# Performance work log

Measured on AMD Instinct MI355X. Metric: run time of the kernel, lower is better.

Reference implementation:

```python
import jax, jax.numpy as jnp
import numpy as np

EPS = 1e-6  # LayerNorm epsilon


def setup_inputs() -> dict:
    key = jax.random.key(0)
    ks = jax.random.split(key, 12)
    B, S, T, E = 8, 2048, 2048, 512
    sc = 1.0 / np.sqrt(E)
    inp = {
        "encoder_outputs": jax.random.normal(ks[0], (B, S, E), jnp.float32),
        "emotion": jax.random.normal(ks[1], (B, T, E), jnp.float32),
        "mask": jax.random.randint(ks[2], (B, S, T), 0, 2).astype(bool),
        "Wq": jax.random.normal(ks[3], (E, E), jnp.float32) * sc,
        "bq": jnp.zeros((E,), jnp.float32),
        "Wk": jax.random.normal(ks[4], (E, E), jnp.float32) * sc,
        "bk": jnp.zeros((E,), jnp.float32),
        "Wv": jax.random.normal(ks[5], (E, E), jnp.float32) * sc,
        "bv": jnp.zeros((E,), jnp.float32),
        "Wo": jax.random.normal(ks[6], (E, E), jnp.float32) * sc,
        "gamma": jnp.ones((E,), jnp.float32),
        "beta": jnp.zeros((E,), jnp.float32),
    }
    return inp


def reference(encoder_outputs, emotion, mask, Wq, bq, Wk, bk, Wv, bv, Wo, gamma, beta):
    # Linear projections (torch Linear: x @ W.T + b)
    q = encoder_outputs @ Wq.T + bq          # [B,S,E]
    k = emotion @ Wk.T + bk                  # [B,T,E]
    v = emotion @ Wv.T + bv                  # [B,T,E]
    logits = jnp.einsum("bse,bte->bst", q, k)  # [B,S,T]
    logits = jnp.where(mask, jnp.float32(-1e18), logits)
    weights = jax.nn.softmax(logits, axis=-1)   # dropout1 = identity (eval)
    contexts = jnp.einsum("bst,bte->bse", weights, v)
    attn = contexts @ Wo.T                   # output_linear, no bias
    attn = encoder_outputs + attn            # dropout2 = identity (eval)
    # LayerNorm (std-based, as in common hand-rolled LayerNorm)
    mean = attn.mean(-1, keepdims=True)
    std = attn.std(-1, keepdims=True)
    context = gamma * (attn - mean) / (std + EPS) + beta
    context = encoder_outputs + context      # dropout3 = identity (eval)
    return context
```

## Files before the change

### kernel.cpp

```cpp
#include <hip/hip_runtime.h>
#include <math.h>
#include <stdint.h>


#define BB 8
#define SS 2048
#define TT 2048
#define EE 512

typedef __attribute__((ext_vector_type(8))) short short8;
typedef __attribute__((ext_vector_type(4))) float f32x4;

__device__ __forceinline__ uint16_t f2bf(float f) {
  uint32_t u = __builtin_bit_cast(uint32_t, f);
  u += 0x7fffu + ((u >> 16) & 1u);
  return (uint16_t)(u >> 16);
}
__device__ __forceinline__ float bf2f(uint16_t h) {
  uint32_t u = ((uint32_t)h) << 16;
  return __builtin_bit_cast(float, u);
}

__device__ __forceinline__ size_t toff(int row, int col, int ld) {
  return (size_t)(row >> 4) * ((size_t)ld << 4) + ((size_t)(col >> 3) << 7)
       + ((row & 15) << 3) + (col & 7);
}

__device__ __forceinline__ void gld16(const void* g, void* l) {
  __builtin_amdgcn_global_load_lds(
      (const __attribute__((address_space(1))) void*)g,
      (__attribute__((address_space(3))) void*)l, 16, 0, 0);
}

template<int ASRC, int BSRC, int EPI, int WN>
__global__ __launch_bounds__(256, 2) void mgemm(
    const void* __restrict__ Ap, const void* __restrict__ Alo,
    const void* __restrict__ Bp, const void* __restrict__ Blo,
    void* __restrict__ Cp, void* __restrict__ C2,
    const float* __restrict__ bias, const float* __restrict__ bias2,
    const float* __restrict__ resid,
    const int* __restrict__ mask, float* __restrict__ sZ,
    int K, int lda, int ldb, int ldc,
    size_t sA, size_t sB, size_t sC, size_t sM)
{
  constexpr bool ALOARR = (ASRC == 0);
  constexpr bool BLOARR = (BSRC == 0);
  constexpr bool T3     = (ASRC == 0) && (BSRC == 0);
  constexpr bool T2     = (ASRC == 0) && (BSRC == 1);
  constexpr int  BN     = 32 * WN;
  constexpr int  ABYTES = ALOARR ? 16384 : 8192;
  constexpr int  BBYTES = BLOARR ? BN * 128 : BN * 64;

  __shared__ char smem[ABYTES + BBYTES];

  const int tid  = threadIdx.x;
  const int lane = tid & 63, wv = tid >> 6;
  const int z    = blockIdx.z;
  const int bm   = blockIdx.y * 128;
  const int bn   = blockIdx.x * BN;
  const int fr   = lane & 15;
  const int wm   = (wv & 1) * 64;
  const int wn   = (wv >> 1) * (16 * WN);

  const f32x4 zero = {0.f, 0.f, 0.f, 0.f};
  f32x4 acc[4][WN];
#pragma unroll
  for (int i = 0; i < 4; ++i)
#pragma unroll
    for (int j = 0; j < WN; ++j) acc[i][j] = zero;

  const size_t loff = (size_t)lane * 8;
  const uint16_t* gAh = (const uint16_t*)Ap + sA * z + (size_t)(bm >> 4) * 16 * lda + loff;
  const uint16_t* gAl = ALOARR ? (const uint16_t*)Alo + sA * z + (size_t)(bm >> 4) * 16 * lda + loff : nullptr;
  const uint16_t* gBh = (const uint16_t*)Bp + sB * z + (size_t)(bn >> 4) * 16 * ldb + loff;
  const uint16_t* gBl = BLOARR ? (const uint16_t*)Blo + sB * z + (size_t)(bn >> 4) * 16 * ldb + loff : nullptr;

  for (int k0 = 0; k0 < K; k0 += 32) {
    const size_t ka = (size_t)k0 * 16;
    __syncthreads();
#pragma unroll
    for (int t = 0; t < 2; ++t) { int s = wv + t * 4;
      gld16(gAh + (size_t)s * 16 * lda + ka, &smem[s * 1024]); }
    if constexpr (ALOARR) {
#pragma unroll
      for (int t = 0; t < 2; ++t) { int s = wv + t * 4;
        gld16(gAl + (size_t)s * 16 * lda + ka, &smem[8192 + s * 1024]); }
    }
#pragma unroll
    for (int t = 0; t < WN / 2; ++t) { int s = wv + t * 4;
      gld16(gBh + (size_t)s * 16 * ldb + ka, &smem[ABYTES + s * 1024]); }
    if constexpr (BLOARR) {
#pragma unroll
      for (int t = 0; t < WN / 2; ++t) { int s = wv + t * 4;
        gld16(gBl + (size_t)s * 16 * ldb + ka, &smem[ABYTES + BN * 64 + s * 1024]); }
    }
    __syncthreads();

    short8 ah[4], bh[WN], al_[4], bl_[WN];
#pragma unroll
    for (int i = 0; i < 4; ++i) {
      const char* p = smem + ((wm >> 4) + i) * 1024 + (lane << 4);
      ah[i] = *(const short8*)p;
      if constexpr (ALOARR) al_[i] = *(const short8*)(p + 8192);
    }
#pragma unroll
    for (int j = 0; j < WN; ++j) {
      const char* p = smem + ABYTES + ((wn >> 4) + j) * 1024 + (lane << 4);
      bh[j] = *(const short8*)p;
      if constexpr (BLOARR) bl_[j] = *(const short8*)(p + BN * 64);
    }
#pragma unroll
    for (int i = 0; i < 4; ++i)
#pragma unroll
      for (int j = 0; j < WN; ++j) {
        acc[i][j] = __builtin_amdgcn_mfma_f32_16x16x32_bf16(ah[i], bh[j], acc[i][j], 0, 0, 0);
        if constexpr (T3) {
          acc[i][j] = __builtin_amdgcn_mfma_f32_16x16x32_bf16(ah[i], bl_[j], acc[i][j], 0, 0, 0);
          acc[i][j] = __builtin_amdgcn_mfma_f32_16x16x32_bf16(al_[i], bh[j], acc[i][j], 0, 0, 0);
        } else if constexpr (T2) {
          acc[i][j] = __builtin_amdgcn_mfma_f32_16x16x32_bf16(al_[i], bh[j], acc[i][j], 0, 0, 0);
        }
      }
  }

  if constexpr (EPI == 5) {
    const unsigned long long* __restrict__ mb = (const unsigned long long*)mask;
    const size_t mrow = (size_t)TT >> 6;
    const size_t mbase = (size_t)z * SS * mrow + ((size_t)(bn + wn) >> 6);
    unsigned long long mw[4][4];
#pragma unroll
    for (int i = 0; i < 4; ++i)
#pragma unroll
      for (int g = 0; g < 4; ++g) {
        const int row = bm + wm + i * 16 + (lane >> 4) * 4 + g;
        mw[i][g] = mb[mbase + (size_t)row * mrow];
      }
#pragma unroll
    for (int i = 0; i < 4; ++i) {
      const int row0 = bm + wm + i * 16 + (lane >> 4) * 4;
#pragma unroll
      for (int g = 0; g < 4; ++g) {
        const int row = row0 + g;
        float rs = 0.f;
#pragma unroll
        for (int j = 0; j < WN; ++j) {
          const int col = bn + wn + j * 16 + fr;
          const bool msk = (mw[i][g] >> (j * 16 + fr)) & 1ull;
          const float e = msk ? 0.f : __expf(acc[i][j][g] - 60.0f);
          ((uint16_t*)Cp)[sC * z + toff(row, col, ldc)] = f2bf(e);
          rs += e;
        }
        rs += __shfl_xor(rs, 1);
        rs += __shfl_xor(rs, 2);
        rs += __shfl_xor(rs, 4);
        rs += __shfl_xor(rs, 8);
        if ((lane & 15) == 0) atomicAdd(&sZ[(size_t)z * SS + row], rs);
      }
    }
  } else {
#pragma unroll
    for (int i = 0; i < 4; ++i) {
      const int row0 = bm + wm + i * 16 + (lane >> 4) * 4;
#pragma unroll
      for (int g = 0; g < 4; ++g) {
        const int row = row0 + g;
        float invZ = 1.0f;
        if constexpr (EPI == 6) invZ = 1.0f / sZ[(size_t)z * SS + row];
#pragma unroll
        for (int j = 0; j < WN; ++j) {
          const int col = bn + wn + j * 16 + fr;
          float v = acc[i][j][g];
          if constexpr (EPI == 0) {
            const float* bp = (z == 0) ? bias : bias2;
            const size_t ci = sC * z + toff(row, col, ldc);
            v += bp[col];
            uint16_t h = f2bf(v);
            ((uint16_t*)Cp)[ci] = h;
            if (z == 0) ((uint16_t*)C2)[ci] = f2bf(v - bf2f(h));
          } else if constexpr (EPI == 1) {
            v += bias[row];
            ((uint16_t*)Cp)[sC * z + toff(row, col, ldc)] = f2bf(v);
          } else if constexpr (EPI == 4) {
            v += resid[(size_t)row * ldc + col];
            ((float*)Cp)[sC * z + (size_t)row * ldc + col] = v;
          } else {
            ((uint16_t*)Cp)[sC * z + toff(row, col, ldc)] = f2bf(v * invZ);
          }
        }
      }
    }
  }
}

__device__ __forceinline__ void split_core(
    const float* __restrict__ x, uint16_t* __restrict__ hi,
    uint16_t* __restrict__ lo, int bid)
{
  __shared__ uint16_t lh[256 * 8 + 16 * 8];
  __shared__ uint16_t ll[256 * 8 + 16 * 8];
  const int t   = threadIdx.x;
  const int seg = bid >> 2, q = bid & 3;

  const float* src = x + (size_t)(seg * 16 + (t >> 4)) * 512 + q * 128 + (t & 15) * 8;
  float4 a = *(const float4*)src;
  float4 b = *(const float4*)(src + 4);
  float v[8] = {a.x, a.y, a.z, a.w, b.x, b.y, b.z, b.w};

  const int slot = (t & 15) * 16 + (t >> 4);
  uint16_t* ph = lh + slot * 8 + (slot >> 4) * 8;
  uint16_t* pl = ll + slot * 8 + (slot >> 4) * 8;
#pragma unroll
  for (int e = 0; e < 8; ++e) {
    uint16_t h = f2bf(v[e]);
    ph[e] = h;
    pl[e] = f2bf(v[e] - bf2f(h));
  }
  __syncthreads();

  const uint16_t* qh = lh + t * 8 + (t >> 4) * 8;
  const uint16_t* ql = ll + t * 8 + (t >> 4) * 8;
  const size_t off = (size_t)seg * 8192 + (size_t)(q * 16 + (t >> 4)) * 128 + (t & 15) * 8;
  *(short8*)(hi + off) = *(const short8*)qh;
  *(short8*)(lo + off) = *(const short8*)ql;
}

__global__ __launch_bounds__(256) void split_pair(
    const float* __restrict__ x0, const float* __restrict__ x1,
    uint16_t* __restrict__ hi, uint16_t* __restrict__ lo, size_t stride,
    const int* __restrict__ mask, unsigned long long* __restrict__ mbits)
{
  if (blockIdx.x >= 8192) {
    const int lane = threadIdx.x & 63;
    const size_t wid = ((size_t)(blockIdx.x - 8192) * 256 + threadIdx.x) >> 6;
    const size_t nwords = (size_t)BB * SS * TT / 64;
    for (size_t w = wid; w < nwords; w += 2048 * 4) {
      const int m = mask[(w << 6) + lane];
      const unsigned long long b = __ballot(m != 0);
      if (lane == 0) mbits[w] = b;
    }
    return;
  }
  const int sel = blockIdx.x >> 12;
  const int bid = blockIdx.x & 4095;
  split_core(sel ? x1 : x0, hi + sel * stride, lo + sel * stride, bid);
}

__global__ __launch_bounds__(256) void split_w4(
    const float* __restrict__ x0, const float* __restrict__ x1,
    const float* __restrict__ x2, const float* __restrict__ x3,
    uint16_t* __restrict__ hi0, uint16_t* __restrict__ lo0, size_t stride)
{
  const int w   = blockIdx.x >> 7;
  const int bid = blockIdx.x & 127;
  const float* x = (w == 0) ? x0 : (w == 1) ? x1 : (w == 2) ? x2 : x3;
  split_core(x, hi0 + w * stride, lo0 + w * stride, bid);
}

__global__ __launch_bounds__(256) void ln_kernel(
    const float* __restrict__ X, const float* __restrict__ enc,
    const float* __restrict__ gamma, const float* __restrict__ beta,
    float* __restrict__ out)
{
  const int row = blockIdx.x * 4 + (threadIdx.x >> 6);
  const int lane = threadIdx.x & 63;
  const size_t base = (size_t)row * EE;
  const int o0 = lane * 4, o1 = 256 + lane * 4;

  float4 x0 = *(const float4*)(X + base + o0);
  float4 x1 = *(const float4*)(X + base + o1);
  float s = x0.x + x0.y + x0.z + x0.w + x1.x + x1.y + x1.z + x1.w;
#pragma unroll
  for (int off = 32; off > 0; off >>= 1) s += __shfl_xor(s, off);
  const float mean = s * (1.0f / 512.0f);

  float d[8] = {x0.x - mean, x0.y - mean, x0.z - mean, x0.w - mean,
                x1.x - mean, x1.y - mean, x1.z - mean, x1.w - mean};
  float s2 = 0.f;
#pragma unroll
  for (int i = 0; i < 8; ++i) s2 = fmaf(d[i], d[i], s2);
#pragma unroll
  for (int off = 32; off > 0; off >>= 1) s2 += __shfl_xor(s2, off);
  const float stdv = sqrtf(s2 * (1.0f / 512.0f));
  const float inv = 1.0f / (stdv + 1e-6f);

  float4 g0 = *(const float4*)(gamma + o0);
  float4 g1 = *(const float4*)(gamma + o1);
  float4 b0 = *(const float4*)(beta + o0);
  float4 b1 = *(const float4*)(beta + o1);
  float4 e0 = *(const float4*)(enc + base + o0);
  float4 e1 = *(const float4*)(enc + base + o1);

  float4 r0, r1;
  r0.x = e0.x + g0.x * d[0] * inv + b0.x;
  r0.y = e0.y + g0.y * d[1] * inv + b0.y;
  r0.z = e0.z + g0.z * d[2] * inv + b0.z;
  r0.w = e0.w + g0.w * d[3] * inv + b0.w;
  r1.x = e1.x + g1.x * d[4] * inv + b1.x;
  r1.y = e1.y + g1.y * d[5] * inv + b1.y;
  r1.z = e1.z + g1.z * d[6] * inv + b1.z;
  r1.w = e1.w + g1.w * d[7] * inv + b1.w;
  *(float4*)(out + base + o0) = r0;
  *(float4*)(out + base + o1) = r1;
}

extern "C" void kernel_launch(void* const* d_in, const int* in_sizes, int n_in,
                              void* d_out, int out_size, void* d_ws, size_t ws_size,
                              hipStream_t stream) {
  const float* enc   = (const float*)d_in[0];
  const float* emo   = (const float*)d_in[1];
  const int*   mask  = (const int*)d_in[2];
  const float* Wq    = (const float*)d_in[3];
  const float* bq    = (const float*)d_in[4];
  const float* Wk    = (const float*)d_in[5];
  const float* bk    = (const float*)d_in[6];
  const float* Wv    = (const float*)d_in[7];
  const float* bv    = (const float*)d_in[8];
  const float* Wo    = (const float*)d_in[9];
  const float* gamma = (const float*)d_in[10];
  const float* beta  = (const float*)d_in[11];
  float* out = (float*)d_out;
  char*  ws  = (char*)d_ws;

  const size_t SZ = (size_t)BB * SS * EE;
  size_t off = 0;
  uint16_t* enc_h = (uint16_t*)(ws + off); off += SZ * 2;
  uint16_t* enc_l = (uint16_t*)(ws + off); off += SZ * 2;
  uint16_t* emo_h = (uint16_t*)(ws + off); off += SZ * 2;
  uint16_t* emo_l = (uint16_t*)(ws + off); off += SZ * 2;
  uint16_t* q_hi  = (uint16_t*)(ws + off); off += SZ * 2;
  uint16_t* q_lo  = (uint16_t*)(ws + off); off += SZ * 2;
  uint16_t* k_hi  = (uint16_t*)(ws + off); off += SZ * 2;
  uint16_t* k_lo  = (uint16_t*)(ws + off); off += SZ * 2;
  uint16_t* vT    = (uint16_t*)(ws + off); off += SZ * 2;
  uint16_t* ctx   = (uint16_t*)(ws + off); off += SZ * 2;
  uint16_t* wq_h  = (uint16_t*)(ws + off); off += EE * EE * 2;
  uint16_t* wq_l  = (uint16_t*)(ws + off); off += EE * EE * 2;
  uint16_t* wk_h  = (uint16_t*)(ws + off); off += EE * EE * 2;
  uint16_t* wk_l  = (uint16_t*)(ws + off); off += EE * EE * 2;
  uint16_t* wv_h  = (uint16_t*)(ws + off); off += EE * EE * 2;
  uint16_t* wv_l  = (uint16_t*)(ws + off); off += EE * EE * 2;
  uint16_t* wo_h  = (uint16_t*)(ws + off); off += EE * EE * 2;
  uint16_t* wo_l  = (uint16_t*)(ws + off); off += EE * EE * 2;
  uint16_t* P_u   = (uint16_t*)(ws + off); off += (size_t)BB * SS * TT * 2;
  float*    sZ    = (float*)(ws + off);    off += (size_t)BB * SS * 4;
  (void)wk_l; (void)wv_l; (void)wo_l;

  unsigned long long* mbits = (unsigned long long*)k_lo;

  const dim3 blk(256);

  split_w4<<<dim3(512), blk, 0, stream>>>(Wq, Wk, Wv, Wo, wq_h, wq_l,
                                          (size_t)2 * EE * EE);
  split_pair<<<dim3(8192 + 2048), blk, 0, stream>>>(enc, emo, enc_h, enc_l,
                                                    (size_t)2 * SZ, mask, mbits);
  hipMemsetAsync(sZ, 0, (size_t)BB * SS * 4, stream);

  mgemm<0, 0, 0, 4><<<dim3(4, 128, 2), blk, 0, stream>>>(
      enc_h, enc_l, wq_h, wq_l, q_hi, q_lo, bq, bk, nullptr, nullptr, nullptr,
      EE, EE, EE, EE, 2 * SZ, (size_t)2 * EE * EE, 2 * SZ, 0);
  mgemm<1, 1, 1, 4><<<dim3(128, 4, 1), blk, 0, stream>>>(
      wv_h, nullptr, emo_h, nullptr, vT, nullptr, bv, nullptr, nullptr,
      nullptr, nullptr, EE, EE, EE, BB * TT, 0, 0, 0, 0);

  mgemm<0, 1, 5, 4><<<dim3(16, 16, 8), blk, 0, stream>>>(
      q_hi, q_lo, k_hi, nullptr, P_u, nullptr, nullptr, nullptr, nullptr,
      (const int*)mbits, sZ, EE, EE, EE, TT,
      (size_t)SS * EE, (size_t)TT * EE, (size_t)SS * TT, 0);

  mgemm<1, 1, 6, 4><<<dim3(4, 16, 8), blk, 0, stream>>>(
      P_u, nullptr, vT, nullptr, ctx, nullptr, nullptr, nullptr, nullptr,
      nullptr, sZ, TT, TT, BB * TT, EE,
      (size_t)SS * TT, (size_t)TT * 16, (size_t)SS * EE, 0);

  mgemm<1, 1, 4, 4><<<dim3(4, 128, 1), blk, 0, stream>>>(
      ctx, nullptr, wo_h, nullptr, out, nullptr, nullptr, nullptr, enc,
      nullptr, nullptr, EE, EE, EE, EE, 0, 0, 0, 0);
  ln_kernel<<<dim3(BB * SS / 4), blk, 0, stream>>>(out, enc, gamma, beta, out);
}
```

Baseline: 542.2 us.

## Fuse input split and mask bit-packing into one vectorized prepass with new bit layout

Replaces the split_pair kernel, which ran separate blocks for the hi/lo bf16 split and for mask packing, with a single prepass in which every block does both jobs. Each block issues wide float4 and int4 loads, packs mask bits with four ballots per int4 so each lane reads 16 contiguous bytes, and writes a permuted bit layout. The EPI==5 logits epilogue is changed to index that new layout with a precomputed shift. The goal is to make the roughly 128 MB mask read and the input split fully coalesced and better overlapped, at the cost of more register use in the prepass and a tightly coupled mask bit format.

```diff
diff --git a/kernel.cpp b/kernel.cpp
--- a/kernel.cpp
+++ b/kernel.cpp
@@ -9,6 +9,7 @@
 #define EE 512
 
 typedef __attribute__((ext_vector_type(8))) short short8;
+typedef __attribute__((ext_vector_type(4))) short short4v;
 typedef __attribute__((ext_vector_type(4))) float f32x4;
 
 __device__ __forceinline__ uint16_t f2bf(float f) {
@@ -125,15 +126,16 @@
 
   if constexpr (EPI == 5) {
     const unsigned long long* __restrict__ mb = (const unsigned long long*)mask;
-    const size_t mrow = (size_t)TT >> 6;
-    const size_t mbase = (size_t)z * SS * mrow + ((size_t)(bn + wn) >> 6);
+    const int c0 = bn + wn;
+    const int sh = ((c0 & 255) >> 2) + (fr >> 2);
+    const size_t mbase = (size_t)z * 65536 + (size_t)((c0 >> 8) << 2) + (fr & 3);
     unsigned long long mw[4][4];
 #pragma unroll
     for (int i = 0; i < 4; ++i)
 #pragma unroll
       for (int g = 0; g < 4; ++g) {
         const int row = bm + wm + i * 16 + (lane >> 4) * 4 + g;
-        mw[i][g] = mb[mbase + (size_t)row * mrow];
+        mw[i][g] = mb[mbase + (size_t)row * 32];
       }
 #pragma unroll
     for (int i = 0; i < 4; ++i) {
@@ -145,7 +147,7 @@
 #pragma unroll
         for (int j = 0; j < WN; ++j) {
           const int col = bn + wn + j * 16 + fr;
-          const bool msk = (mw[i][g] >> (j * 16 + fr)) & 1ull;
+          const bool msk = (mw[i][g] >> (sh + j * 4)) & 1ull;
           const float e = msk ? 0.f : __expf(acc[i][j][g] - 60.0f);
           ((uint16_t*)Cp)[sC * z + toff(row, col, ldc)] = f2bf(e);
           rs += e;
@@ -224,25 +226,61 @@
   *(short8*)(lo + off) = *(const short8*)ql;
 }
 
-__global__ __launch_bounds__(256) void split_pair(
-    const float* __restrict__ x0, const float* __restrict__ x1,
+__global__ __launch_bounds__(256) void prepass(
+    const float* __restrict__ enc, const float* __restrict__ emo,
     uint16_t* __restrict__ hi, uint16_t* __restrict__ lo, size_t stride,
     const int* __restrict__ mask, unsigned long long* __restrict__ mbits)
 {
-  if (blockIdx.x >= 8192) {
-    const int lane = threadIdx.x & 63;
-    const size_t wid = ((size_t)(blockIdx.x - 8192) * 256 + threadIdx.x) >> 6;
-    const size_t nwords = (size_t)BB * SS * TT / 64;
-    for (size_t w = wid; w < nwords; w += 2048 * 4) {
-      const int m = mask[(w << 6) + lane];
-      const unsigned long long b = __ballot(m != 0);
-      if (lane == 0) mbits[w] = b;
-    }
-    return;
+  const int t    = threadIdx.x;
+  const int lane = t & 63, wv = t >> 6;
+  const int arr  = blockIdx.x >> 10;
+  const int lb   = blockIdx.x & 1023;
+
+  const float* src = (arr ? emo : enc);
+  float4 f[8];
+#pragma unroll
+  for (int r = 0; r < 8; ++r)
+    f[r] = *((const float4*)src + (size_t)lb * 2048 + r * 256 + t);
+
+  const int4* mp = (const int4*)mask + (size_t)blockIdx.x * 4096;
+  int4 m[16];
+#pragma unroll
+  for (int r = 0; r < 16; ++r)
+    m[r] = mp[r * 256 + t];
+
+  uint16_t* hp = hi + (size_t)arr * stride;
+  uint16_t* lp = lo + (size_t)arr * stride;
+#pragma unroll
+  for (int r = 0; r < 8; ++r) {
+    const int lf  = lb * 2048 + r * 256 + t;
+    const int row = lf >> 7;
+    const int k   = (lf & 127) * 4;
+    const size_t off = (size_t)(row >> 4) * 8192 + (size_t)(k >> 3) * 128
+                     + (row & 15) * 8 + (k & 7);
+    const float v[4] = {f[r].x, f[r].y, f[r].z, f[r].w};
+    short4v hv, lv;
+#pragma unroll
+    for (int e = 0; e < 4; ++e) {
+      const uint16_t h = f2bf(v[e]);
+      hv[e] = (short)h;
+      lv[e] = (short)f2bf(v[e] - bf2f(h));
+    }
+    *(short4v*)(hp + off) = hv;
+    *(short4v*)(lp + off) = lv;
   }
-  const int sel = blockIdx.x >> 12;
-  const int bid = blockIdx.x & 4095;
-  split_core(sel ? x1 : x0, hi + sel * stride, lo + sel * stride, bid);
+
+#pragma unroll
+  for (int r = 0; r < 16; ++r) {
+    const unsigned long long b0 = __ballot(m[r].x != 0);
+    const unsigned long long b1 = __ballot(m[r].y != 0);
+    const unsigned long long b2 = __ballot(m[r].z != 0);
+    const unsigned long long b3 = __ballot(m[r].w != 0);
+    if (lane < 4) {
+      const unsigned long long w = (lane == 0) ? b0 : (lane == 1) ? b1
+                                 : (lane == 2) ? b2 : b3;
+      mbits[(size_t)blockIdx.x * 256 + r * 16 + wv * 4 + lane] = w;
+    }
+  }
 }
 
 __global__ __launch_bounds__(256) void split_w4(
@@ -351,8 +389,8 @@
 
   split_w4<<<dim3(512), blk, 0, stream>>>(Wq, Wk, Wv, Wo, wq_h, wq_l,
                                           (size_t)2 * EE * EE);
-  split_pair<<<dim3(8192 + 2048), blk, 0, stream>>>(enc, emo, enc_h, enc_l,
-                                                    (size_t)2 * SZ, mask, mbits);
+  prepass<<<dim3(2048), blk, 0, stream>>>(enc, emo, enc_h, enc_l,
+                                          (size_t)2 * SZ, mask, mbits);
   hipMemsetAsync(sZ, 0, (size_t)BB * SS * 4, stream);
 
   mgemm<0, 0, 0, 4><<<dim3(4, 128, 2), blk, 0, stream>>>(
```

Measured after the change: 556.9 us. 1.03x slower.
